# Kernel optimization log

Hardware: AMD Instinct MI355X
Metric: run time of the kernel (lower is better)

The kernel has to match this reference:

```python
import jax, jax.numpy as jnp
import numpy as np

BN_EPS = 1e-5

def _bn(x, p):
    # p: [4, C] = (gamma, beta, running_mean, running_var); inference-mode BN
    g, b, m, v = p[0], p[1], p[2], p[3]
    if x.ndim == 3:  # [B, C, N]
        g, b, m, v = g[:, None], b[:, None], m[:, None], v[:, None]
    return g * (x - m) * jax.lax.rsqrt(v + BN_EPS) + b

def _angle_density(xyz, npoints=32):
    # xyz: [B, N, 3]; pairwise cosine distance via a single GEMM instead of expand
    inner = jnp.einsum('bnc,bmc->bnm', xyz, xyz)            # [B, N, N]
    nrm = jnp.sqrt(jnp.sum(xyz * xyz, axis=-1))             # [B, N]
    dist = 1.0 - inner / (nrm[:, :, None] * nrm[:, None, :])
    neg_vals, _ = jax.lax.top_k(-dist, npoints)             # k smallest distances
    feat_density = jnp.mean(-neg_vals, axis=-1)             # [B, N]
    inv = 1.0 / feat_density
    return inv / jnp.max(inv)                               # global max, as in torch

def _density_attn(x, density, wqk, wt, bt, bnp):
    # x: [B, C, N]; density: [B, 1, N]; wqk: [C//4, 1] (q_conv and k_conv share weights)
    xk = wqk * density                                      # [B, C//4, N] (1x1 conv, 1 in-ch)
    energy = jnp.einsum('bdn,bdm->bnm', xk, xk)             # x_q == x_k.T (shared weight)
    attn = jax.nn.softmax(energy, axis=-1)
    attn = attn / (1e-9 + jnp.sum(attn, axis=1, keepdims=True))
    x_r = jnp.einsum('bcn,bnm->bcm', x, attn)               # [B, C, N]
    y = jnp.einsum('oc,bcn->bon', wt, x - x_r) + bt[:, None]
    return x + jax.nn.relu(_bn(y, bnp))

def _conv_bn_relu(x, w, bnp):
    return jax.nn.relu(_bn(jnp.einsum('oc,bcn->bon', w, x), bnp))

def _forward(x, w1, w2, w3, w4, w5, bn1, bn2, bn3, bn4, bn5,
             da1_wqk, da1_wt, da1_bt, da1_bn,
             da2_wqk, da2_wt, da2_bt, da2_bn,
             da3_wqk, da3_wt, da3_bt, da3_bn,
             da4_wqk, da4_wt, da4_bt, da4_bn,
             lin1_w, bn6, lin2_w, lin2_b):
    dens = _angle_density(jnp.transpose(x, (0, 2, 1)), 32)[:, None, :]  # [B, 1, N]
    h = _conv_bn_relu(x, w1, bn1)
    h = _density_attn(h, dens, da1_wqk, da1_wt, da1_bt, da1_bn)
    h = _conv_bn_relu(h, w2, bn2)
    h = _density_attn(h, dens, da2_wqk, da2_wt, da2_bt, da2_bn)
    h = _conv_bn_relu(h, w3, bn3)
    h = _density_attn(h, dens, da3_wqk, da3_wt, da3_bt, da3_bn)
    h = _conv_bn_relu(h, w4, bn4)
    h = _density_attn(h, dens, da4_wqk, da4_wt, da4_bt, da4_bn)
    h = _conv_bn_relu(h, w5, bn5)                           # [B, 1024, N]
    h = jnp.max(h, axis=-1)                                 # adaptive_max_pool1d -> [B, 1024]
    h = jax.nn.relu(_bn(h @ lin1_w.T, bn6))                 # [B, 512]; dropout is identity in eval
    return h @ lin2_w.T + lin2_b                            # [B, num_classes]

def setup_inputs() -> dict:
    key = jax.random.key(0)
    ki = iter(jax.random.split(key, 80))
    def rn(shape, s):
        return jax.random.normal(next(ki), shape, jnp.float32) * s
    def bnp(c):
        return jnp.stack([
            jax.random.uniform(next(ki), (c,), jnp.float32, 0.5, 1.5),  # gamma
            rn((c,), 0.05),                                             # beta
            rn((c,), 0.1),                                              # running_mean
            jax.random.uniform(next(ki), (c,), jnp.float32, 0.5, 1.5),  # running_var
        ])
    B, N, E = 16, 2048, 1024
    d = {}
    d['x'] = jax.random.normal(next(ki), (B, 3, N), jnp.float32)
    d['w1'] = rn((64, 3), 0.5)
    d['w2'] = rn((64, 64), 0.125)
    d['w3'] = rn((64, 64), 0.125)
    d['w4'] = rn((128, 64), 0.125)
    d['w5'] = rn((E, 128), 0.09)
    d['bn1'], d['bn2'], d['bn3'] = bnp(64), bnp(64), bnp(64)
    d['bn4'], d['bn5'] = bnp(128), bnp(E)
    for i, c in zip((1, 2, 3, 4), (64, 64, 64, 128)):
        d[f'da{i}_wqk'] = rn((c // 4, 1), 1.0)
        d[f'da{i}_wt'] = rn((c, c), 1.0 / np.sqrt(c))
        d[f'da{i}_bt'] = rn((c,), 0.05)
        d[f'da{i}_bn'] = bnp(c)
    d['lin1_w'] = rn((512, E), 1.0 / np.sqrt(E))
    d['bn6'] = bnp(512)
    d['lin2_w'] = rn((40, 512), 1.0 / np.sqrt(512))
    d['lin2_b'] = rn((40,), 0.05)
    return d

def reference(x, w1, w2, w3, w4, w5, bn1, bn2, bn3, bn4, bn5,
              da1_wqk, da1_wt, da1_bt, da1_bn,
              da2_wqk, da2_wt, da2_bt, da2_bn,
              da3_wqk, da3_wt, da3_bt, da3_bn,
              da4_wqk, da4_wt, da4_bt, da4_bn,
              lin1_w, bn6, lin2_w, lin2_b):
    return _forward(x, w1, w2, w3, w4, w5, bn1, bn2, bn3, bn4, bn5,
                    da1_wqk, da1_wt, da1_bt, da1_bn,
                    da2_wqk, da2_wt, da2_bt, da2_bn,
                    da3_wqk, da3_wt, da3_bt, da3_bn,
                    da4_wqk, da4_wt, da4_bt, da4_bn,
                    lin1_w, bn6, lin2_w, lin2_b)
```

## Files before the change

### kernel.cpp

```cpp
#include <hip/hip_runtime.h>
#include <math.h>

#define BB 16
#define NN 2048
#define BN_EPS_ 1e-5f

typedef __attribute__((ext_vector_type(8))) short short8v;
typedef __attribute__((ext_vector_type(4))) float f32x4;

__device__ __forceinline__ unsigned short f2bf(float x){
  unsigned u = __float_as_uint(x);
  u += 0x7fffu + ((u >> 16) & 1u);
  return (unsigned short)(u >> 16);
}
__device__ __forceinline__ float bf2f(unsigned short h){
  return __uint_as_float(((unsigned)h) << 16);
}

__global__ __launch_bounds__(256) void normalize_points_kernel(const float* __restrict__ x,
        float* __restrict__ u){
  int idx = blockIdx.x*256 + threadIdx.x;
  int b = idx >> 11, n = idx & (NN-1);
  const float* xb = x + (size_t)b*3*NN;
  float x0 = xb[n], x1 = xb[NN+n], x2 = xb[2*NN+n];
  float rn = rsqrtf(x0*x0 + x1*x1 + x2*x2);
  float* ub = u + (size_t)b*3*NN;
  ub[n] = x0*rn; ub[NN+n] = x1*rn; ub[2*NN+n] = x2*rn;
}

#define DG 8
__global__ __launch_bounds__(256) void density6_kernel(const float* __restrict__ u,
        float* __restrict__ inv, float* __restrict__ blockmax){
  __shared__ float us0[NN], us1[NN], us2[NN];
  __shared__ unsigned int hist[DG][256];
  __shared__ float buf[DG][128];
  __shared__ unsigned int bufcnt[DG];
  __shared__ unsigned int bB[DG], bC0[DG];
  __shared__ float partial[DG][4];
  __shared__ float rowiv[DG];
  const int b = blockIdx.y;
  const float* ub = u + (size_t)b*3*NN;
  const int t = threadIdx.x;
  #pragma unroll
  for (int i = 0; i < NN/(256*4); ++i){
    int n4 = t + 256*i;
    ((float4*)us0)[n4] = ((const float4*)ub)[n4];
    ((float4*)us1)[n4] = ((const float4*)(ub+NN))[n4];
    ((float4*)us2)[n4] = ((const float4*)(ub+2*NN))[n4];
  }
  #pragma unroll
  for (int i = 0; i < DG; ++i) hist[i][t & 255] = 0u;
  if (t < DG) bufcnt[t] = 0u;
  __syncthreads();
  float m0[8], m1[8], m2[8];
  #pragma unroll
  for (int i = 0; i < 8; ++i){
    int c = t + 256*i;
    m0[i] = us0[c]; m1[i] = us1[c]; m2[i] = us2[c];
  }
  const int r0 = blockIdx.x * DG;
  float ru0[DG], ru1[DG], ru2[DG];
  #pragma unroll
  for (int j = 0; j < DG; ++j){ ru0[j] = us0[r0+j]; ru1[j] = us1[r0+j]; ru2[j] = us2[r0+j]; }

  float dd[DG][8];
  unsigned qp[DG][2];
  #pragma unroll
  for (int j = 0; j < DG; ++j){
    unsigned q0 = 0u, q1 = 0u;
    #pragma unroll
    for (int i = 0; i < 8; ++i){
      float d = 1.0f - (ru0[j]*m0[i] + ru1[j]*m1[i] + ru2[j]*m2[i]);
      dd[j][i] = d;
      int q = (int)(d * 128.0f);
      q = q < 0 ? 0 : (q > 255 ? 255 : q);
      if (i < 4) q0 |= (unsigned)q << (8*i); else q1 |= (unsigned)q << (8*(i-4));
      atomicAdd(&hist[j][q], 1u);
    }
    qp[j][0] = q0; qp[j][1] = q1;
  }
  __syncthreads();

  const int wave = t >> 6, lane = t & 63;
  #pragma unroll
  for (int jj = 0; jj < 2; ++jj){
    const int j = 2*wave + jj;
    uint4 cc = *(const uint4*)&hist[j][lane*4];
    unsigned tl = cc.x + cc.y + cc.z + cc.w;
    unsigned inc = tl;
    #pragma unroll
    for (int off = 1; off < 64; off <<= 1){
      unsigned o = __shfl_up(inc, off);
      if (lane >= off) inc += o;
    }
    unsigned base = inc - tl;
    if (base < 32u && base + tl >= 32u){
      unsigned cum = base;
      if (cum < 32u && cum + cc.x >= 32u){ bB[j] = lane*4 + 0; bC0[j] = cum; } cum += cc.x;
      if (cum < 32u && cum + cc.y >= 32u){ bB[j] = lane*4 + 1; bC0[j] = cum; } cum += cc.y;
      if (cum < 32u && cum + cc.z >= 32u){ bB[j] = lane*4 + 2; bC0[j] = cum; } cum += cc.z;
      if (cum < 32u && cum + cc.w >= 32u){ bB[j] = lane*4 + 3; bC0[j] = cum; } cum += cc.w;
    }
  }
  __syncthreads();

  #pragma unroll
  for (int j = 0; j < DG; ++j){
    const int B = (int)bB[j];
    float s = 0.0f;
    #pragma unroll
    for (int i = 0; i < 8; ++i){
      float d = dd[j][i];
      const int q = (int)((qp[j][i>>2] >> (8*(i&3))) & 255u);
      if (q < B) s += d;
      else if (q == B){
        unsigned slot = atomicAdd(&bufcnt[j], 1u);
        if (slot < 128u) buf[j][slot] = d;
      }
    }
    #pragma unroll
    for (int off = 32; off > 0; off >>= 1) s += __shfl_xor(s, off);
    if (lane == 0) partial[j][wave] = s;
  }
  __syncthreads();

  #pragma unroll
  for (int jj = 0; jj < 2; ++jj){
    const int j = 2*wave + jj;
    float total = partial[j][0] + partial[j][1] + partial[j][2] + partial[j][3];
    int cnt = (int)bufcnt[j]; if (cnt > 128) cnt = 128;
    const int rr = 32 - (int)bC0[j];
    float v1 = (lane      < cnt) ? buf[j][lane]      : 0.0f;
    float v2 = (lane + 64 < cnt) ? buf[j][lane + 64] : 0.0f;
    int rk1 = 0, rk2 = 0;
    for (int k = 0; k < cnt; ++k){
      float vk = buf[j][k];
      rk1 += ((vk < v1) || (vk == v1 && k < lane)) ? 1 : 0;
      rk2 += ((vk < v2) || (vk == v2 && k < lane + 64)) ? 1 : 0;
    }
    float contrib = ((lane      < cnt) && (rk1 < rr)) ? v1 : 0.0f;
    contrib      += ((lane + 64 < cnt) && (rk2 < rr)) ? v2 : 0.0f;
    #pragma unroll
    for (int off = 32; off > 0; off >>= 1) contrib += __shfl_xor(contrib, off);
    total += contrib;
    if (lane == 0){
      float iv = 32.0f / total;
      inv[b*NN + r0 + j] = iv;
      rowiv[j] = iv;
    }
  }
  __syncthreads();
  if (t == 0){
    float m = rowiv[0];
    #pragma unroll
    for (int j = 1; j < DG; ++j) m = fmaxf(m, rowiv[j]);
    blockmax[blockIdx.y * gridDim.x + blockIdx.x] = m;
  }
}

__global__ __launch_bounds__(256) void finalize_max_kernel(const float* __restrict__ blockmax,
        float* __restrict__ maxout){
  __shared__ float pw[4];
  const int t = threadIdx.x;
  float m = 0.0f;
  #pragma unroll
  for (int i = 0; i < 16; ++i) m = fmaxf(m, blockmax[t + 256*i]);
  #pragma unroll
  for (int off = 32; off > 0; off >>= 1) m = fmaxf(m, __shfl_xor(m, off));
  if ((t & 63) == 0) pw[t >> 6] = m;
  __syncthreads();
  if (t == 0) *maxout = fmaxf(fmaxf(pw[0], pw[1]), fmaxf(pw[2], pw[3]));
}

__global__ void normalize_kernel(float* __restrict__ dens, const float* __restrict__ maxval){
  int i = blockIdx.x*256 + threadIdx.x;
  float mx = *maxval;
  dens[i] = dens[i] / mx;
}

__global__ __launch_bounds__(256) void zrow_kernel(const float* __restrict__ dens,
      const float* __restrict__ wqk, int K, float* __restrict__ out){
  __shared__ float ds[NN];
  const int b = blockIdx.y, t = threadIdx.x;
  float s = 0.0f;
  for (int k = 0; k < K; ++k){ float w = wqk[k]; s += w*w; }
  #pragma unroll
  for (int i = 0; i < NN/256; ++i) ds[t + 256*i] = dens[b*NN + t + 256*i];
  __syncthreads();
  const int wave = t >> 6, lane = t & 63;
  const int RPB = NN / gridDim.x;
  const int r0 = blockIdx.x * RPB;
  for (int r = r0 + wave; r < r0 + RPB; r += 4){
    float a = s * ds[r];
    float sum = 0.0f;
    #pragma unroll
    for (int i = 0; i < NN/64; ++i){
      int m = lane + 64*i;
      sum += __expf(a * ds[m]);
    }
    #pragma unroll
    for (int off = 32; off > 0; off >>= 1) sum += __shfl_xor(sum, off);
    if (lane == 0) out[b*NN + r] = 1.0f/sum;
  }
}

template<int C>
__global__ __launch_bounds__(256, 2) void attn_mfma_kernel(const unsigned short* __restrict__ Ah,
      const unsigned short* __restrict__ Al, const float* __restrict__ dens,
      const float* __restrict__ zinv, const float* __restrict__ wqk, int K,
      unsigned short* __restrict__ raw){
  constexpr int RA = C + 16;
  constexpr int RH = C / 32;
  __shared__ __align__(16) unsigned short ah[C][64], al[C][64];
  __shared__ __align__(16) unsigned short eh[64][64];
  const int id = blockIdx.x;
  const int b  = (id & 7) + ((id >> 9) << 3);
  const int inner = (id >> 3) & 63;
  const int m0 = (inner & 31) * 64;
  const int nh = inner >> 5;
  const size_t HS = (size_t)BB*RA*NN;
  const int t = threadIdx.x;
  float s = 0.0f;
  for (int k = 0; k < K; ++k){ float w = wqk[k]; s += w*w; }
  const float* db = dens + b*NN;
  const float* zb = zinv + b*NN;
  const unsigned short* Abh = Ah + (size_t)b*C*NN;
  const unsigned short* Abl = Al + (size_t)b*C*NN;
  const int ej = t >> 2, ekq = (t & 3) * 16;
  const float dmj = s * db[m0 + ej];
  const unsigned swe = (unsigned)((ej & 7) << 4);
  const int l = t & 63, w = t >> 6;
  const int rw = w & 1, cw = w >> 1;
  const int fc = l & 15, g = l >> 4;
  const unsigned swr = (unsigned)((fc & 7) << 4);
  short8v ones8, zero8;
  #pragma unroll
  for (int q = 0; q < 8; ++q){ ones8[q] = (short)0x3F80; zero8[q] = 0; }
  f32x4 acc[RH][2], cs[2];
  #pragma unroll
  for (int i = 0; i < RH; ++i){ acc[i][0] = (f32x4){0.f,0.f,0.f,0.f}; acc[i][1] = (f32x4){0.f,0.f,0.f,0.f}; }
  cs[0] = (f32x4){0.f,0.f,0.f,0.f}; cs[1] = (f32x4){0.f,0.f,0.f,0.f};

  for (int n0 = nh*(NN/2); n0 < (nh+1)*(NN/2); n0 += 64){
    __syncthreads();
    #pragma unroll
    for (int i = 0; i < C*8/256; ++i){
      int idx = t + 256*i;
      int row = idx >> 3, c8 = (idx & 7) * 8;
      unsigned off = (unsigned)(row*128) + (((unsigned)(c8*2)) ^ ((unsigned)((row&7)<<4)));
      *(uint4*)((char*)ah + off) = *(const uint4*)(Abh + (size_t)row*NN + n0 + c8);
      *(uint4*)((char*)al + off) = *(const uint4*)(Abl + (size_t)row*NN + n0 + c8);
    }
    {
      unsigned hp[8];
      #pragma unroll
      for (int u = 0; u < 4; ++u){
        float4 dn = *(const float4*)(db + n0 + ekq + u*4);
        float4 zv = *(const float4*)(zb + n0 + ekq + u*4);
        float e0 = zv.x*__expf(dn.x*dmj), e1 = zv.y*__expf(dn.y*dmj);
        float e2 = zv.z*__expf(dn.z*dmj), e3 = zv.w*__expf(dn.w*dmj);
        hp[u*2+0] = (unsigned)f2bf(e0) | ((unsigned)f2bf(e1)<<16);
        hp[u*2+1] = (unsigned)f2bf(e2) | ((unsigned)f2bf(e3)<<16);
      }
      unsigned row = (unsigned)(ej*128);
      unsigned o1 = row + (((unsigned)(ekq*2))      ^ swe);
      unsigned o2 = row + (((unsigned)(ekq*2 + 16)) ^ swe);
      *(uint4*)((char*)eh + o1) = make_uint4(hp[0],hp[1],hp[2],hp[3]);
      *(uint4*)((char*)eh + o2) = make_uint4(hp[4],hp[5],hp[6],hp[7]);
    }
    __syncthreads();
    #pragma unroll
    for (int kk = 0; kk < 2; ++kk){
      unsigned ko = ((unsigned)((kk*32 + g*8)*2)) ^ swr;
      short8v bh[2], ai[RH], au[RH];
      #pragma unroll
      for (int ct = 0; ct < 2; ++ct){
        unsigned eoff = (unsigned)(((2*cw + ct)*16 + fc)*128) + ko;
        bh[ct] = *(const short8v*)((const char*)eh + eoff);
      }
      #pragma unroll
      for (int i = 0; i < RH; ++i){
        unsigned aoff = (unsigned)((rw*(C/2) + i*16 + fc)*128) + ko;
        ai[i] = *(const short8v*)((const char*)ah + aoff);
        au[i] = *(const short8v*)((const char*)al + aoff);
      }
      __builtin_amdgcn_s_setprio(1);
      #pragma unroll
      for (int i = 0; i < RH; ++i){
        #pragma unroll
        for (int ct = 0; ct < 2; ++ct){
          acc[i][ct] = __builtin_amdgcn_mfma_f32_16x16x32_bf16(ai[i], bh[ct], acc[i][ct], 0, 0, 0);
          acc[i][ct] = __builtin_amdgcn_mfma_f32_16x16x32_bf16(au[i], bh[ct], acc[i][ct], 0, 0, 0);
        }
      }
      if (rw == 1){
        short8v ac = (fc == 0) ? ones8 : zero8;
        #pragma unroll
        for (int ct = 0; ct < 2; ++ct)
          cs[ct] = __builtin_amdgcn_mfma_f32_16x16x32_bf16(ac, bh[ct], cs[ct], 0, 0, 0);
      }
      __builtin_amdgcn_s_setprio(0);
    }
  }
  #pragma unroll
  for (int ct = 0; ct < 2; ++ct){
    unsigned short* rb = raw + (size_t)nh*HS + (size_t)b*RA*NN + m0 + (2*cw + ct)*16 + fc;
    #pragma unroll
    for (int i = 0; i < RH; ++i){
      #pragma unroll
      for (int r = 0; r < 4; ++r){
        int row = rw*(C/2) + i*16 + g*4 + r;
        rb[(size_t)row*NN] = f2bf(acc[i][ct][r]);
      }
    }
    if (rw == 1){
      #pragma unroll
      for (int r = 0; r < 4; ++r){
        int row = C + g*4 + r;
        rb[(size_t)row*NN] = f2bf(cs[ct][r]);
      }
    }
  }
}

template<int C, bool TP>
__global__ __launch_bounds__(256) void attn_post_kernel(const float* __restrict__ x,
      const unsigned short* __restrict__ raw, const float* __restrict__ wt,
      const float* __restrict__ bt, const float* __restrict__ bnp,
      float* __restrict__ out, unsigned short* __restrict__ th,
      unsigned short* __restrict__ tl){
  constexpr int RA = C + 16;
  __shared__ float ds[32][68];
  __shared__ float ws[32][C+4];
  __shared__ float cbs[64];
  const int b = blockIdx.y, m0 = blockIdx.x*64, t = threadIdx.x;
  const size_t HS = (size_t)BB*RA*NN;
  const float* xb = x + (size_t)b*C*NN;
  const unsigned short* rb0 = raw + (size_t)b*RA*NN;
  const unsigned short* rb1 = raw + HS + (size_t)b*RA*NN;
  if (t < 64) cbs[t] = 1.0f / (1e-9f + bf2f(rb0[(size_t)C*NN + m0 + t]) + bf2f(rb1[(size_t)C*NN + m0 + t]));
  const int tr = t >> 4, tc = t & 15;
  constexpr int R = C/16;
  float acc[R][4];
  #pragma unroll
  for (int i = 0; i < R; ++i){ acc[i][0]=acc[i][1]=acc[i][2]=acc[i][3]=0.0f; }
  for (int c0 = 0; c0 < C; c0 += 32){
    __syncthreads();
    #pragma unroll
    for (int i = 0; i < 8; ++i){
      int idx = t + 256*i;
      int m = idx & 63, cl = idx >> 6;
      int cc = c0 + cl;
      float rv = bf2f(rb0[cc*NN + m0 + m]) + bf2f(rb1[cc*NN + m0 + m]);
      ds[cl][m] = xb[cc*NN + m0 + m] - rv * cbs[m];
    }
    #pragma unroll
    for (int i = 0; i < C*32/256; ++i){
      int idx = t + 256*i;
      int cl = idx & 31, o = idx >> 5;
      ws[cl][o] = wt[o*C + c0 + cl];
    }
    __syncthreads();
    #pragma unroll
    for (int k = 0; k < 32; ++k){
      float4 e = *(const float4*)&ds[k][tc*4];
      float a[R];
      #pragma unroll
      for (int q = 0; q < R/4; ++q)
        *(float4*)&a[q*4] = *(const float4*)&ws[k][tr*R + q*4];
      #pragma unroll
      for (int i = 0; i < R; ++i){
        acc[i][0] += a[i]*e.x; acc[i][1] += a[i]*e.y;
        acc[i][2] += a[i]*e.z; acc[i][3] += a[i]*e.w;
      }
    }
  }
  #pragma unroll
  for (int i = 0; i < R; ++i){
    int o = tr*R + i;
    float g = bnp[o], be = bnp[C+o], mn = bnp[2*C+o], vv = bnp[3*C+o];
    float sc = g * rsqrtf(vv + BN_EPS_);
    float sh = be - mn*sc;
    float bv = bt[o];
    #pragma unroll
    for (int j = 0; j < 4; ++j){
      float y = acc[i][j] + bv;
      y = sc*y + sh;
      y = fmaxf(y, 0.0f);
      acc[i][j] = xb[o*NN + m0 + tc*4 + j] + y;
    }
    if (!TP)
      *(float4*)&out[((size_t)b*C + o)*NN + m0 + tc*4] =
          make_float4(acc[i][0], acc[i][1], acc[i][2], acc[i][3]);
  }
  if (TP){
    unsigned short* Ts = (unsigned short*)&ws[0][0];
    #pragma unroll
    for (int pass = 0; pass < 2; ++pass){
      __syncthreads();
      #pragma unroll
      for (int q = 0; q < R/2; ++q){
        #pragma unroll
        for (int j = 0; j < 4; ++j){
          int n = tc*4 + j;
          float y0 = acc[2*q][j], y1 = acc[2*q+1][j];
          unsigned short a0 = f2bf(y0), a1 = f2bf(y1);
          unsigned short v0 = pass ? f2bf(y0 - bf2f(a0)) : a0;
          unsigned short v1 = pass ? f2bf(y1 - bf2f(a1)) : a1;
          unsigned off = (unsigned)(n*256) +
              (((unsigned)((tr*R + 2*q)*2)) ^ ((unsigned)((n&7)<<4)));
          *(unsigned*)((char*)Ts + off) = (unsigned)v0 | ((unsigned)v1<<16);
        }
      }
      __syncthreads();
      unsigned short* gout = (pass ? tl : th) + ((size_t)b*NN + m0)*128;
      int n = t >> 2;
      #pragma unroll
      for (int s2 = 0; s2 < 4; ++s2){
        int sl = (t&3)*4 + s2;
        unsigned off = (unsigned)(n*256) + ((unsigned)((sl ^ (n&7)) << 4));
        uint4 v = *(const uint4*)((const char*)Ts + off);
        *(uint4*)(gout + (size_t)n*128 + sl*8) = v;
      }
    }
  }
}

template<int CIN, int COUT>
__global__ __launch_bounds__(256) void conv_bn_relu_kernel(const float* __restrict__ x,
      const float* __restrict__ w, const float* __restrict__ bnp, float* __restrict__ out,
      unsigned short* __restrict__ oh, unsigned short* __restrict__ ol){
  constexpr int CH = (CIN < 32) ? CIN : 32;
  __shared__ float xs[CH][68];
  __shared__ float ws[CH][COUT+4];
  const int b = blockIdx.y, m0 = blockIdx.x*64, t = threadIdx.x;
  const float* xb = x + (size_t)b*CIN*NN;
  const int tr = t >> 4, tc = t & 15;
  constexpr int R = COUT/16;
  float acc[R][4];
  #pragma unroll
  for (int i = 0; i < R; ++i){ acc[i][0]=acc[i][1]=acc[i][2]=acc[i][3]=0.0f; }
  for (int c0 = 0; c0 < CIN; c0 += CH){
    __syncthreads();
    for (int idx = t; idx < CH*64; idx += 256){
      int m = idx & 63, cl = idx >> 6;
      xs[cl][m] = xb[(c0+cl)*NN + m0 + m];
    }
    for (int idx = t; idx < CH*COUT; idx += 256){
      int cl = idx % CH, o = idx / CH;
      ws[cl][o] = w[o*CIN + c0 + cl];
    }
    __syncthreads();
    #pragma unroll
    for (int k = 0; k < CH; ++k){
      float4 e = *(const float4*)&xs[k][tc*4];
      float a[R];
      #pragma unroll
      for (int q = 0; q < R/4; ++q)
        *(float4*)&a[q*4] = *(const float4*)&ws[k][tr*R + q*4];
      #pragma unroll
      for (int i = 0; i < R; ++i){
        acc[i][0] += a[i]*e.x; acc[i][1] += a[i]*e.y;
        acc[i][2] += a[i]*e.z; acc[i][3] += a[i]*e.w;
      }
    }
  }
  #pragma unroll
  for (int i = 0; i < R; ++i){
    int o = tr*R + i;
    float g = bnp[o], be = bnp[COUT+o], mn = bnp[2*COUT+o], vv = bnp[3*COUT+o];
    float sc = g * rsqrtf(vv + BN_EPS_);
    float sh = be - mn*sc;
    float4 r;
    float* rp = &r.x;
    #pragma unroll
    for (int j = 0; j < 4; ++j){
      float y = sc*acc[i][j] + sh;
      rp[j] = fmaxf(y, 0.0f);
    }
    size_t base = ((size_t)b*COUT + o)*NN + m0 + tc*4;
    *(float4*)&out[base] = r;
    unsigned short h0=f2bf(r.x), h1=f2bf(r.y), h2=f2bf(r.z), h3=f2bf(r.w);
    uint2 hp, lp;
    hp.x = (unsigned)h0 | ((unsigned)h1<<16);
    hp.y = (unsigned)h2 | ((unsigned)h3<<16);
    lp.x = (unsigned)f2bf(r.x-bf2f(h0)) | ((unsigned)f2bf(r.y-bf2f(h1))<<16);
    lp.y = (unsigned)f2bf(r.z-bf2f(h2)) | ((unsigned)f2bf(r.w-bf2f(h3))<<16);
    *(uint2*)&oh[base] = hp;
    *(uint2*)&ol[base] = lp;
  }
}

__global__ __launch_bounds__(256, 2) void conv5_mfma_kernel(
      const unsigned short* __restrict__ hTh, const unsigned short* __restrict__ hTl,
      const float* __restrict__ w5, const float* __restrict__ bnp,
      float* __restrict__ pooled){
  __shared__ __align__(16) unsigned short wh[64][128], wl[64][128];
  __shared__ __align__(16) unsigned short hh[64][128], hl[64][128];
  const int id = blockIdx.x;
  const int b  = (id & 7) + ((id >> 9) << 3);
  const int inner = (id >> 3) & 63;
  const int o0 = (inner & 15) * 64;
  const int nb = (inner >> 4) * (NN/4);
  const int t = threadIdx.x;
  const int l = t & 63, w = t >> 6;
  const int rw = w & 1, cw = w >> 1;
  const int fc = l & 15, g = l >> 4;
  const unsigned swr = (unsigned)((fc & 7) << 4);
  #pragma unroll
  for (int i = 0; i < 8; ++i){
    int idx = t + 256*i;
    int row = idx >> 5, c0 = (idx & 31) * 4;
    float4 v = *(const float4*)(w5 + (size_t)(o0 + row)*128 + c0);
    unsigned short h0=f2bf(v.x), h1=f2bf(v.y), h2=f2bf(v.z), h3=f2bf(v.w);
    uint2 hp, lp;
    hp.x = (unsigned)h0 | ((unsigned)h1<<16);
    hp.y = (unsigned)h2 | ((unsigned)h3<<16);
    lp.x = (unsigned)f2bf(v.x-bf2f(h0)) | ((unsigned)f2bf(v.y-bf2f(h1))<<16);
    lp.y = (unsigned)f2bf(v.z-bf2f(h2)) | ((unsigned)f2bf(v.w-bf2f(h3))<<16);
    unsigned off = (unsigned)(row*256) + (((unsigned)(c0*2)) ^ ((unsigned)((row&7)<<4)));
    *(uint2*)((char*)wh + off) = hp;
    *(uint2*)((char*)wl + off) = lp;
  }
  float sc[2][4], sh[2][4];
  #pragma unroll
  for (int i = 0; i < 2; ++i){
    #pragma unroll
    for (int r = 0; r < 4; ++r){
      int o = o0 + rw*32 + i*16 + g*4 + r;
      float gg = bnp[o], be = bnp[1024+o], mn = bnp[2048+o], vv = bnp[3072+o];
      sc[i][r] = gg * rsqrtf(vv + BN_EPS_);
      sh[i][r] = be - mn*sc[i][r];
    }
  }
  float vmax[2][4] = {{0.f,0.f,0.f,0.f},{0.f,0.f,0.f,0.f}};
  const unsigned short* hb = hTh + (size_t)b*NN*128;
  const unsigned short* lb = hTl + (size_t)b*NN*128;
  for (int nt = 0; nt < (NN/4)/64; ++nt){
    const int n0 = nb + nt*64;
    __syncthreads();
    #pragma unroll
    for (int i = 0; i < 4; ++i){
      int idx = t + 256*i;
      int row = idx >> 4, sl = idx & 15;
      unsigned off = (unsigned)(row*256) + ((unsigned)((sl << 4) ^ ((row&7)<<4)));
      *(uint4*)((char*)hh + off) = *(const uint4*)(hb + (size_t)(n0+row)*128 + sl*8);
      *(uint4*)((char*)hl + off) = *(const uint4*)(lb + (size_t)(n0+row)*128 + sl*8);
    }
    __syncthreads();
    f32x4 acc[2][2];
    #pragma unroll
    for (int i = 0; i < 2; ++i){ acc[i][0] = (f32x4){0.f,0.f,0.f,0.f}; acc[i][1] = (f32x4){0.f,0.f,0.f,0.f}; }
    #pragma unroll
    for (int kk = 0; kk < 4; ++kk){
      unsigned ko = ((unsigned)((kk*32 + g*8)*2)) ^ swr;
      short8v aih[2], ail[2], bih[2], bil[2];
      #pragma unroll
      for (int i = 0; i < 2; ++i){
        unsigned aoff = (unsigned)((rw*32 + i*16 + fc)*256) + ko;
        aih[i] = *(const short8v*)((const char*)wh + aoff);
        ail[i] = *(const short8v*)((const char*)wl + aoff);
      }
      #pragma unroll
      for (int ct = 0; ct < 2; ++ct){
        unsigned boff = (unsigned)((cw*32 + ct*16 + fc)*256) + ko;
        bih[ct] = *(const short8v*)((const char*)hh + boff);
        bil[ct] = *(const short8v*)((const char*)hl + boff);
      }
      #pragma unroll
      for (int i = 0; i < 2; ++i){
        #pragma unroll
        for (int ct = 0; ct < 2; ++ct){
          acc[i][ct] = __builtin_amdgcn_mfma_f32_16x16x32_bf16(aih[i], bih[ct], acc[i][ct], 0, 0, 0);
          acc[i][ct] = __builtin_amdgcn_mfma_f32_16x16x32_bf16(aih[i], bil[ct], acc[i][ct], 0, 0, 0);
          acc[i][ct] = __builtin_amdgcn_mfma_f32_16x16x32_bf16(ail[i], bih[ct], acc[i][ct], 0, 0, 0);
        }
      }
    }
    #pragma unroll
    for (int i = 0; i < 2; ++i){
      #pragma unroll
      for (int ct = 0; ct < 2; ++ct){
        #pragma unroll
        for (int r = 0; r < 4; ++r){
          float y = sc[i][r]*acc[i][ct][r] + sh[i][r];
          y = fmaxf(y, 0.0f);
          vmax[i][r] = fmaxf(vmax[i][r], y);
        }
      }
    }
  }
  #pragma unroll
  for (int i = 0; i < 2; ++i){
    #pragma unroll
    for (int r = 0; r < 4; ++r){
      float v = vmax[i][r];
      v = fmaxf(v, __shfl_xor(v, 1));
      v = fmaxf(v, __shfl_xor(v, 2));
      v = fmaxf(v, __shfl_xor(v, 4));
      v = fmaxf(v, __shfl_xor(v, 8));
      if (fc == 0)
        atomicMax((unsigned int*)&pooled[b*1024 + o0 + rw*32 + i*16 + g*4 + r],
                  __float_as_uint(v));
    }
  }
}

__global__ void lin1_kernel(const float* __restrict__ pooled, const float* __restrict__ w,
      const float* __restrict__ bnp, float* __restrict__ out1){
  int tid = blockIdx.x*256 + threadIdx.x;
  int b = tid >> 9, j = tid & 511;
  const float4* p4 = (const float4*)(pooled + b*1024);
  const float4* w4 = (const float4*)(w + j*1024);
  float sum = 0.0f;
  for (int e = 0; e < 256; ++e){
    float4 a = p4[e], c = w4[e];
    sum += a.x*c.x + a.y*c.y + a.z*c.z + a.w*c.w;
  }
  float g = bnp[j], be = bnp[512+j], mn = bnp[2*512+j], vv = bnp[3*512+j];
  float s = g * rsqrtf(vv + BN_EPS_);
  float y = s*sum + (be - mn*s);
  out1[b*512 + j] = fmaxf(y, 0.0f);
}

__global__ void lin2_kernel(const float* __restrict__ h, const float* __restrict__ w,
      const float* __restrict__ bias, float* __restrict__ out){
  int tid = blockIdx.x*64 + threadIdx.x;
  if (tid >= 640) return;
  int b = tid / 40, k = tid % 40;
  const float4* h4 = (const float4*)(h + b*512);
  const float4* w4 = (const float4*)(w + k*512);
  float sum = 0.0f;
  for (int e = 0; e < 128; ++e){
    float4 a = h4[e], c = w4[e];
    sum += a.x*c.x + a.y*c.y + a.z*c.z + a.w*c.w;
  }
  out[tid] = sum + bias[k];
}

extern "C" void kernel_launch(void* const* d_in, const int* in_sizes, int n_in,
                              void* d_out, int out_size, void* d_ws, size_t ws_size,
                              hipStream_t stream){
  (void)in_sizes; (void)n_in; (void)out_size; (void)ws_size;
  const float* x     = (const float*)d_in[0];
  const float* w1    = (const float*)d_in[1];
  const float* w2    = (const float*)d_in[2];
  const float* w3    = (const float*)d_in[3];
  const float* w4    = (const float*)d_in[4];
  const float* w5    = (const float*)d_in[5];
  const float* bn1   = (const float*)d_in[6];
  const float* bn2   = (const float*)d_in[7];
  const float* bn3   = (const float*)d_in[8];
  const float* bn4   = (const float*)d_in[9];
  const float* bn5   = (const float*)d_in[10];
  const float* da_wqk[4] = {(const float*)d_in[11], (const float*)d_in[15], (const float*)d_in[19], (const float*)d_in[23]};
  const float* da_wt[4]  = {(const float*)d_in[12], (const float*)d_in[16], (const float*)d_in[20], (const float*)d_in[24]};
  const float* da_bt[4]  = {(const float*)d_in[13], (const float*)d_in[17], (const float*)d_in[21], (const float*)d_in[25]};
  const float* da_bn[4]  = {(const float*)d_in[14], (const float*)d_in[18], (const float*)d_in[22], (const float*)d_in[26]};
  const float* lin1_w = (const float*)d_in[27];
  const float* bn6    = (const float*)d_in[28];
  const float* lin2_w = (const float*)d_in[29];
  const float* lin2_b = (const float*)d_in[30];

  float* ws = (float*)d_ws;
  float* maxval = ws;
  float* dens   = ws + 64;
  float* zinv   = dens + BB*NN;
  float* hA     = zinv + BB*NN;
  float* hB     = hA  + (size_t)BB*64*NN;
  float* h4A    = hB  + (size_t)BB*64*NN;
  unsigned short* raw = (unsigned short*)(h4A + (size_t)BB*128*NN);
  float* pooled = (float*)raw + (size_t)BB*144*NN;
  float* l1o    = pooled + BB*1024;
  float* uvec   = l1o + BB*512;
  float* blockmax = uvec + (size_t)BB*3*NN;
  unsigned short* Ah = (unsigned short*)(blockmax + 4096);
  unsigned short* Al = Ah + (size_t)BB*128*NN;
  float* h4B    = hA;

  normalize_points_kernel<<<dim3(BB*NN/256), 256, 0, stream>>>(x, uvec);
  density6_kernel<<<dim3(NN/DG, BB), 256, 0, stream>>>(uvec, dens, blockmax);
  finalize_max_kernel<<<dim3(1), 256, 0, stream>>>(blockmax, maxval);
  normalize_kernel<<<dim3(BB*NN/256), 256, 0, stream>>>(dens, maxval);

  conv_bn_relu_kernel<3,64><<<dim3(32,BB),256,0,stream>>>(x, w1, bn1, hA, Ah, Al);

  zrow_kernel<<<dim3(32,BB),256,0,stream>>>(dens, da_wqk[0], 16, zinv);
  attn_mfma_kernel<64><<<dim3(1024),256,0,stream>>>(Ah, Al, dens, zinv, da_wqk[0], 16, raw);
  attn_post_kernel<64,false><<<dim3(32,BB),256,0,stream>>>(hA, raw, da_wt[0], da_bt[0], da_bn[0], hB, nullptr, nullptr);

  conv_bn_relu_kernel<64,64><<<dim3(32,BB),256,0,stream>>>(hB, w2, bn2, hA, Ah, Al);

  zrow_kernel<<<dim3(32,BB),256,0,stream>>>(dens, da_wqk[1], 16, zinv);
  attn_mfma_kernel<64><<<dim3(1024),256,0,stream>>>(Ah, Al, dens, zinv, da_wqk[1], 16, raw);
  attn_post_kernel<64,false><<<dim3(32,BB),256,0,stream>>>(hA, raw, da_wt[1], da_bt[1], da_bn[1], hB, nullptr, nullptr);

  conv_bn_relu_kernel<64,64><<<dim3(32,BB),256,0,stream>>>(hB, w3, bn3, hA, Ah, Al);

  zrow_kernel<<<dim3(32,BB),256,0,stream>>>(dens, da_wqk[2], 16, zinv);
  attn_mfma_kernel<64><<<dim3(1024),256,0,stream>>>(Ah, Al, dens, zinv, da_wqk[2], 16, raw);
  attn_post_kernel<64,false><<<dim3(32,BB),256,0,stream>>>(hA, raw, da_wt[2], da_bt[2], da_bn[2], hB, nullptr, nullptr);

  conv_bn_relu_kernel<64,128><<<dim3(32,BB),256,0,stream>>>(hB, w4, bn4, h4A, Ah, Al);

  zrow_kernel<<<dim3(32,BB),256,0,stream>>>(dens, da_wqk[3], 32, zinv);
  attn_mfma_kernel<128><<<dim3(1024),256,0,stream>>>(Ah, Al, dens, zinv, da_wqk[3], 32, raw);
  attn_post_kernel<128,true><<<dim3(32,BB),256,0,stream>>>(h4A, raw, da_wt[3], da_bt[3], da_bn[3], h4B, Ah, Al);

  hipMemsetAsync(pooled, 0, BB*1024*sizeof(float), stream);
  conv5_mfma_kernel<<<dim3(1024),256,0,stream>>>(Ah, Al, w5, bn5, pooled);
  lin1_kernel<<<dim3(32),256,0,stream>>>(pooled, lin1_w, bn6, l1o);
  lin2_kernel<<<dim3(10),64,0,stream>>>(l1o, lin2_w, lin2_b, (float*)d_out);
}
```

Measured before the change: 539.5 us.

## Fuse point normalization into density kernel and batch softmax row sums

Folds the point-normalization pass into the density kernel, which now runs 512 threads per block so each thread handles 4 columns. The separate normalize-by-max kernel is removed by folding 1/max² into the attention scale. The four per-layer zrow launches are merged into one kernel that computes all four row-sum inverses in a single pass over density. This removes several small launches and memory round-trips, at the cost of larger per-thread exp work in the merged zrow kernel and 4x zinv storage.

```diff
diff --git a/kernel.cpp b/kernel.cpp
--- a/kernel.cpp
+++ b/kernel.cpp
@@ -17,74 +17,65 @@
   return __uint_as_float(((unsigned)h) << 16);
 }
 
-__global__ __launch_bounds__(256) void normalize_points_kernel(const float* __restrict__ x,
-        float* __restrict__ u){
-  int idx = blockIdx.x*256 + threadIdx.x;
-  int b = idx >> 11, n = idx & (NN-1);
-  const float* xb = x + (size_t)b*3*NN;
-  float x0 = xb[n], x1 = xb[NN+n], x2 = xb[2*NN+n];
-  float rn = rsqrtf(x0*x0 + x1*x1 + x2*x2);
-  float* ub = u + (size_t)b*3*NN;
-  ub[n] = x0*rn; ub[NN+n] = x1*rn; ub[2*NN+n] = x2*rn;
-}
-
 #define DG 8
-__global__ __launch_bounds__(256) void density6_kernel(const float* __restrict__ u,
+__global__ __launch_bounds__(512) void density7_kernel(const float* __restrict__ x,
         float* __restrict__ inv, float* __restrict__ blockmax){
   __shared__ float us0[NN], us1[NN], us2[NN];
   __shared__ unsigned int hist[DG][256];
   __shared__ float buf[DG][128];
   __shared__ unsigned int bufcnt[DG];
   __shared__ unsigned int bB[DG], bC0[DG];
-  __shared__ float partial[DG][4];
+  __shared__ float partial[DG][8];
   __shared__ float rowiv[DG];
   const int b = blockIdx.y;
-  const float* ub = u + (size_t)b*3*NN;
+  const float* xb = x + (size_t)b*3*NN;
   const int t = threadIdx.x;
-  #pragma unroll
-  for (int i = 0; i < NN/(256*4); ++i){
-    int n4 = t + 256*i;
-    ((float4*)us0)[n4] = ((const float4*)ub)[n4];
-    ((float4*)us1)[n4] = ((const float4*)(ub+NN))[n4];
-    ((float4*)us2)[n4] = ((const float4*)(ub+2*NN))[n4];
-  }
-  #pragma unroll
-  for (int i = 0; i < DG; ++i) hist[i][t & 255] = 0u;
+  {
+    float4 v0 = ((const float4*)xb)[t];
+    float4 v1 = ((const float4*)(xb + NN))[t];
+    float4 v2 = ((const float4*)(xb + 2*NN))[t];
+    float4 rr;
+    rr.x = rsqrtf(v0.x*v0.x + v1.x*v1.x + v2.x*v2.x);
+    rr.y = rsqrtf(v0.y*v0.y + v1.y*v1.y + v2.y*v2.y);
+    rr.z = rsqrtf(v0.z*v0.z + v1.z*v1.z + v2.z*v2.z);
+    rr.w = rsqrtf(v0.w*v0.w + v1.w*v1.w + v2.w*v2.w);
+    v0.x*=rr.x; v0.y*=rr.y; v0.z*=rr.z; v0.w*=rr.w;
+    v1.x*=rr.x; v1.y*=rr.y; v1.z*=rr.z; v1.w*=rr.w;
+    v2.x*=rr.x; v2.y*=rr.y; v2.z*=rr.z; v2.w*=rr.w;
+    ((float4*)us0)[t] = v0; ((float4*)us1)[t] = v1; ((float4*)us2)[t] = v2;
+  }
+  #pragma unroll
+  for (int i = 0; i < 4; ++i) ((unsigned*)hist)[t + 512*i] = 0u;
   if (t < DG) bufcnt[t] = 0u;
   __syncthreads();
-  float m0[8], m1[8], m2[8];
-  #pragma unroll
-  for (int i = 0; i < 8; ++i){
-    int c = t + 256*i;
+  float m0[4], m1[4], m2[4];
+  #pragma unroll
+  for (int i = 0; i < 4; ++i){
+    int c = t + 512*i;
     m0[i] = us0[c]; m1[i] = us1[c]; m2[i] = us2[c];
   }
   const int r0 = blockIdx.x * DG;
-  float ru0[DG], ru1[DG], ru2[DG];
-  #pragma unroll
-  for (int j = 0; j < DG; ++j){ ru0[j] = us0[r0+j]; ru1[j] = us1[r0+j]; ru2[j] = us2[r0+j]; }
-
-  float dd[DG][8];
-  unsigned qp[DG][2];
+  float dd[DG][4]; unsigned qp[DG];
   #pragma unroll
   for (int j = 0; j < DG; ++j){
-    unsigned q0 = 0u, q1 = 0u;
-    #pragma unroll
-    for (int i = 0; i < 8; ++i){
-      float d = 1.0f - (ru0[j]*m0[i] + ru1[j]*m1[i] + ru2[j]*m2[i]);
+    float ru0 = us0[r0+j], ru1 = us1[r0+j], ru2 = us2[r0+j];
+    unsigned q0 = 0u;
+    #pragma unroll
+    for (int i = 0; i < 4; ++i){
+      float d = 1.0f - (ru0*m0[i] + ru1*m1[i] + ru2*m2[i]);
       dd[j][i] = d;
       int q = (int)(d * 128.0f);
       q = q < 0 ? 0 : (q > 255 ? 255 : q);
-      if (i < 4) q0 |= (unsigned)q << (8*i); else q1 |= (unsigned)q << (8*(i-4));
+      q0 |= (unsigned)q << (8*i);
       atomicAdd(&hist[j][q], 1u);
     }
-    qp[j][0] = q0; qp[j][1] = q1;
+    qp[j] = q0;
   }
   __syncthreads();
 
   const int wave = t >> 6, lane = t & 63;
-  #pragma unroll
-  for (int jj = 0; jj < 2; ++jj){
-    const int j = 2*wave + jj;
+  {
+    const int j = wave;
     uint4 cc = *(const uint4*)&hist[j][lane*4];
     unsigned tl = cc.x + cc.y + cc.z + cc.w;
     unsigned inc = tl;
@@ -109,9 +100,9 @@
     const int B = (int)bB[j];
     float s = 0.0f;
     #pragma unroll
-    for (int i = 0; i < 8; ++i){
+    for (int i = 0; i < 4; ++i){
       float d = dd[j][i];
-      const int q = (int)((qp[j][i>>2] >> (8*(i&3))) & 255u);
+      int q = (int)((qp[j] >> (8*i)) & 255u);
       if (q < B) s += d;
       else if (q == B){
         unsigned slot = atomicAdd(&bufcnt[j], 1u);
@@ -124,10 +115,11 @@
   }
   __syncthreads();
 
-  #pragma unroll
-  for (int jj = 0; jj < 2; ++jj){
-    const int j = 2*wave + jj;
-    float total = partial[j][0] + partial[j][1] + partial[j][2] + partial[j][3];
+  {
+    const int j = wave;
+    float total = 0.0f;
+    #pragma unroll
+    for (int wv = 0; wv < 8; ++wv) total += partial[j][wv];
     int cnt = (int)bufcnt[j]; if (cnt > 128) cnt = 128;
     const int rr = 32 - (int)bC0[j];
     float v1 = (lane      < cnt) ? buf[j][lane]      : 0.0f;
@@ -172,18 +164,21 @@
   if (t == 0) *maxout = fmaxf(fmaxf(pw[0], pw[1]), fmaxf(pw[2], pw[3]));
 }
 
-__global__ void normalize_kernel(float* __restrict__ dens, const float* __restrict__ maxval){
-  int i = blockIdx.x*256 + threadIdx.x;
-  float mx = *maxval;
-  dens[i] = dens[i] / mx;
-}
-
-__global__ __launch_bounds__(256) void zrow_kernel(const float* __restrict__ dens,
-      const float* __restrict__ wqk, int K, float* __restrict__ out){
+__global__ __launch_bounds__(256) void zrow4_kernel(const float* __restrict__ dens,
+      const float* __restrict__ maxval,
+      const float* __restrict__ w0, const float* __restrict__ w1,
+      const float* __restrict__ w2, const float* __restrict__ w3,
+      float* __restrict__ out){
   __shared__ float ds[NN];
   const int b = blockIdx.y, t = threadIdx.x;
-  float s = 0.0f;
-  for (int k = 0; k < K; ++k){ float w = wqk[k]; s += w*w; }
+  float mx = *maxval;
+  float r2 = 1.0f / (mx*mx);
+  float s0=0.f, s1=0.f, s2=0.f, s3=0.f;
+  for (int k = 0; k < 16; ++k){ float w = w0[k]; s0 += w*w; }
+  for (int k = 0; k < 16; ++k){ float w = w1[k]; s1 += w*w; }
+  for (int k = 0; k < 16; ++k){ float w = w2[k]; s2 += w*w; }
+  for (int k = 0; k < 32; ++k){ float w = w3[k]; s3 += w*w; }
+  s0 *= r2; s1 *= r2; s2 *= r2; s3 *= r2;
   #pragma unroll
   for (int i = 0; i < NN/256; ++i) ds[t + 256*i] = dens[b*NN + t + 256*i];
   __syncthreads();
@@ -191,16 +186,26 @@
   const int RPB = NN / gridDim.x;
   const int r0 = blockIdx.x * RPB;
   for (int r = r0 + wave; r < r0 + RPB; r += 4){
-    float a = s * ds[r];
-    float sum = 0.0f;
+    float dr = ds[r];
+    float a0 = s0*dr, a1 = s1*dr, a2 = s2*dr, a3 = s3*dr;
+    float q0=0.f, q1=0.f, q2=0.f, q3=0.f;
     #pragma unroll
     for (int i = 0; i < NN/64; ++i){
-      int m = lane + 64*i;
-      sum += __expf(a * ds[m]);
-    }
-    #pragma unroll
-    for (int off = 32; off > 0; off >>= 1) sum += __shfl_xor(sum, off);
-    if (lane == 0) out[b*NN + r] = 1.0f/sum;
+      float dm = ds[lane + 64*i];
+      q0 += __expf(a0*dm); q1 += __expf(a1*dm);
+      q2 += __expf(a2*dm); q3 += __expf(a3*dm);
+    }
+    #pragma unroll
+    for (int off = 32; off > 0; off >>= 1){
+      q0 += __shfl_xor(q0, off); q1 += __shfl_xor(q1, off);
+      q2 += __shfl_xor(q2, off); q3 += __shfl_xor(q3, off);
+    }
+    if (lane == 0){
+      out[0*(size_t)BB*NN + b*NN + r] = 1.0f/q0;
+      out[1*(size_t)BB*NN + b*NN + r] = 1.0f/q1;
+      out[2*(size_t)BB*NN + b*NN + r] = 1.0f/q2;
+      out[3*(size_t)BB*NN + b*NN + r] = 1.0f/q3;
+    }
   }
 }
 
@@ -208,7 +213,7 @@
 __global__ __launch_bounds__(256, 2) void attn_mfma_kernel(const unsigned short* __restrict__ Ah,
       const unsigned short* __restrict__ Al, const float* __restrict__ dens,
       const float* __restrict__ zinv, const float* __restrict__ wqk, int K,
-      unsigned short* __restrict__ raw){
+      const float* __restrict__ maxval, unsigned short* __restrict__ raw){
   constexpr int RA = C + 16;
   constexpr int RH = C / 32;
   __shared__ __align__(16) unsigned short ah[C][64], al[C][64];
@@ -222,6 +227,7 @@
   const int t = threadIdx.x;
   float s = 0.0f;
   for (int k = 0; k < K; ++k){ float w = wqk[k]; s += w*w; }
+  { float mx = *maxval; s = s / (mx*mx); }
   const float* db = dens + b*NN;
   const float* zb = zinv + b*NN;
   const unsigned short* Abh = Ah + (size_t)b*C*NN;
@@ -665,46 +671,41 @@
   float* ws = (float*)d_ws;
   float* maxval = ws;
   float* dens   = ws + 64;
-  float* zinv   = dens + BB*NN;
-  float* hA     = zinv + BB*NN;
+  float* zinv4  = dens + BB*NN;
+  float* hA     = zinv4 + 4*(size_t)BB*NN;
   float* hB     = hA  + (size_t)BB*64*NN;
   float* h4A    = hB  + (size_t)BB*64*NN;
   unsigned short* raw = (unsigned short*)(h4A + (size_t)BB*128*NN);
   float* pooled = (float*)raw + (size_t)BB*144*NN;
   float* l1o    = pooled + BB*1024;
-  float* uvec   = l1o + BB*512;
-  float* blockmax = uvec + (size_t)BB*3*NN;
+  float* blockmax = l1o + BB*512;
   unsigned short* Ah = (unsigned short*)(blockmax + 4096);
   unsigned short* Al = Ah + (size_t)BB*128*NN;
   float* h4B    = hA;
 
-  normalize_points_kernel<<<dim3(BB*NN/256), 256, 0, stream>>>(x, uvec);
-  density6_kernel<<<dim3(NN/DG, BB), 256, 0, stream>>>(uvec, dens, blockmax);
+  density7_kernel<<<dim3(NN/DG, BB), 512, 0, stream>>>(x, dens, blockmax);
   finalize_max_kernel<<<dim3(1), 256, 0, stream>>>(blockmax, maxval);
-  normalize_kernel<<<dim3(BB*NN/256), 256, 0, stream>>>(dens, maxval);
+  zrow4_kernel<<<dim3(32,BB), 256, 0, stream>>>(dens, maxval,
+      da_wqk[0], da_wqk[1], da_wqk[2], da_wqk[3], zinv4);
 
   conv_bn_relu_kernel<3,64><<<dim3(32,BB),256,0,stream>>>(x, w1, bn1, hA, Ah, Al);
 
-  zrow_kernel<<<dim3(32,BB),256,0,stream>>>(dens, da_wqk[0], 16, zinv);
-  attn_mfma_kernel<64><<<dim3(1024),256,0,stream>>>(Ah, Al, dens, zinv, da_wqk[0], 16, raw);
+  attn_mfma_kernel<64><<<dim3(1024),256,0,stream>>>(Ah, Al, dens, zinv4, da_wqk[0], 16, maxval, raw);
   attn_post_kernel<64,false><<<dim3(32,BB),256,0,stream>>>(hA, raw, da_wt[0], da_bt[0], da_bn[0], hB, nullptr, nullptr);
 
   conv_bn_relu_kernel<64,64><<<dim3(32,BB),256,0,stream>>>(hB, w2, bn2, hA, Ah, Al);
 
-  zrow_kernel<<<dim3(32,BB),256,0,stream>>>(dens, da_wqk[1], 16, zinv);
-  attn_mfma_kernel<64><<<dim3(1024),256,0,stream>>>(Ah, Al, dens, zinv, da_wqk[1], 16, raw);
+  attn_mfma_kernel<64><<<dim3(1024),256,0,stream>>>(Ah, Al, dens, zinv4 + (size_t)BB*NN, da_wqk[1], 16, maxval, raw);
   attn_post_kernel<64,false><<<dim3(32,BB),256,0,stream>>>(hA, raw, da_wt[1], da_bt[1], da_bn[1], hB, nullptr, nullptr);
 
   conv_bn_relu_kernel<64,64><<<dim3(32,BB),256,0,stream>>>(hB, w3, bn3, hA, Ah, Al);
 
-  zrow_kernel<<<dim3(32,BB),256,0,stream>>>(dens, da_wqk[2], 16, zinv);
-  attn_mfma_kernel<64><<<dim3(1024),256,0,stream>>>(Ah, Al, dens, zinv, da_wqk[2], 16, raw);
+  attn_mfma_kernel<64><<<dim3(1024),256,0,stream>>>(Ah, Al, dens, zinv4 + 2*(size_t)BB*NN, da_wqk[2], 16, maxval, raw);
   attn_post_kernel<64,false><<<dim3(32,BB),256,0,stream>>>(hA, raw, da_wt[2], da_bt[2], da_bn[2], hB, nullptr, nullptr);
 
   conv_bn_relu_kernel<64,128><<<dim3(32,BB),256,0,stream>>>(hB, w4, bn4, h4A, Ah, Al);
 
-  zrow_kernel<<<dim3(32,BB),256,0,stream>>>(dens, da_wqk[3], 32, zinv);
-  attn_mfma_kernel<128><<<dim3(1024),256,0,stream>>>(Ah, Al, dens, zinv, da_wqk[3], 32, raw);
+  attn_mfma_kernel<128><<<dim3(1024),256,0,stream>>>(Ah, Al, dens, zinv4 + 3*(size_t)BB*NN, da_wqk[3], 32, maxval, raw);
   attn_post_kernel<128,true><<<dim3(32,BB),256,0,stream>>>(h4A, raw, da_wt[3], da_bt[3], da_bn[3], h4B, Ah, Al);
 
   hipMemsetAsync(pooled, 0, BB*1024*sizeof(float), stream);
```

New measurement: 498.3 us (median of 2 runs). 1.08x faster.
